# Kernel tuning notes

Measured on AMD Instinct MI355X. Metric: run time of the kernel, lower is better.

The kernel has to match this reference:

```python
import jax, jax.numpy as jnp
import numpy as np

# --- constants from init_kwargs / module defaults ---
H, W, C = 720, 1280, 2
T_EVT, T_PROP = 10, 10
T_TOTAL = T_EVT + T_PROP          # 20 temporal steps (10 event + 10 propagation)
TAU, THR0 = 10.0, 1.0             # LIF time constant, base threshold
ALPHA, TARGET_RATE = 0.1, 0.1     # PENT adaptation
THR_MIN, THR_MAX = 0.1, 10.0
N_EVENTS = 4_000_000


def setup_inputs() -> dict:
    key = jax.random.key(0)
    k1, k2, k3, k4 = jax.random.split(key, 4)
    x = jax.random.randint(k1, (N_EVENTS,), 0, W, dtype=jnp.int32)
    y = jax.random.randint(k2, (N_EVENTS,), 0, H, dtype=jnp.int32)
    p = jax.random.randint(k3, (N_EVENTS,), 0, 2, dtype=jnp.int32)
    t = jax.random.uniform(k4, (N_EVENTS,), dtype=jnp.float32)
    return {"x": x, "y": y, "p": p, "t": t}


def _build_buffer(x, y, p, t):
    # TemporalBuffer.forward: bin events into first T_EVT steps, rest are zeros.
    tmin, tmax = t.min(), t.max()
    denom = jnp.where(tmax > tmin, tmax - tmin, jnp.float32(1.0))
    t_norm = jnp.where(tmax > tmin, (t - tmin) / denom * (T_EVT - 1e-6), 0.0)
    t_idx = jnp.clip(t_norm.astype(jnp.int32), 0, T_EVT - 1)
    xi = jnp.clip(x, 0, W - 1)
    yi = jnp.clip(y, 0, H - 1)
    c_idx = p  # p in {0,1} -> channel index directly (p.min() >= 0 branch)
    buf = jnp.zeros((T_TOTAL, C, H, W), jnp.float32)
    return buf.at[t_idx, c_idx, yi, xi].add(1.0)


def reference(x, y, p, t):
    buffer = _build_buffer(x, y, p, t)  # (T, C, H, W)
    decay = jnp.float32(np.exp(-1.0 / TAU))

    def step(carry, frame):
        mem, thr = carry
        # LIFBuffer: decay + accumulate
        mem = mem * decay + frame
        spk = (mem >= thr).astype(jnp.float32)
        mem = mem - spk * thr  # soft ('subtract') reset
        # AdaptiveThreshold (PENT): homeostatic rate-based adaptation
        rate = spk.mean()
        thr = jnp.clip(thr + ALPHA * (rate - TARGET_RATE), THR_MIN, THR_MAX)
        return (mem, thr), spk

    mem0 = jnp.zeros((C, H, W), jnp.float32)
    (_, _), spikes = jax.lax.scan(step, (mem0, jnp.float32(THR0)), buffer)
    return spikes  # (T, C, H, W) binary spike activity maps
```

## Files before the change

### kernel.cpp

```cpp
#include <hip/hip_runtime.h>
#include <cstddef>

#define HH 720
#define WW 1280
#define FRAME 1843200
#define FRAME4 460800
#define T_EVT 10
#define T_TOTAL 20
#define ARRIVE64 (1ULL << 32)

#define ONBLK 256
#define ONTHR 1024
#define ONWPB 16
#define ONT (ONBLK * ONTHR)

#define SBLK 1024
#define STHR 256
#define SWPB 4
#define PIXB 1800
#define NGROUP4 450
#define HIST_W 9000
#define RBLK 512
#define RTHR 1024
#define OTHR 512
#define NBUCKET 1024
#define BBLK (RBLK / 2)
#define EPT 20
#define MAXM (EPT * RTHR)

#define MAT_OFF   0u
#define CS_OFF    (512u * 1024u * 4u)
#define SB_OFF    (CS_OFF + 4096u)
#define KEY_OFF   (SB_OFF + 8192u)
#define SEG_OFF(n) (KEY_OFF + 4u * (unsigned)(n))
#define WS_NEED(n) ((size_t)SEG_OFF(n) + 2ull * (size_t)(n) + 256ull)

__device__ unsigned g_minkey;
__device__ unsigned g_maxkey;
__device__ unsigned g_part_mn[RBLK];
__device__ unsigned g_part_mx[RBLK];
__device__ unsigned long long g_grp[T_TOTAL][16][16];
__device__ unsigned long long g_top[T_TOTAL][16];
__device__ unsigned g_rel[T_TOTAL][32];
__device__ unsigned long long g_n1[T_TOTAL][64][16];
__device__ unsigned long long g_n2[T_TOTAL][4][16];
__device__ unsigned long long g_n3[T_TOTAL][16];
__device__ unsigned g_relg[T_TOTAL][64][32];

__device__ __forceinline__ unsigned f2key(float f) {
    unsigned b = __float_as_uint(f);
    return b ^ ((unsigned)(((int)b) >> 31) | 0x80000000u);
}
__device__ __forceinline__ float key2f(unsigned k) {
    unsigned b = (k & 0x80000000u) ? (k ^ 0x80000000u) : ~k;
    return __uint_as_float(b);
}

__device__ __forceinline__ int event_bin_t(float tv, float tmin, float tmax) {
#pragma clang fp contract(off)
    float tn;
    if (tmax > tmin) tn = (tv - tmin) / (tmax - tmin) * (float)(10.0 - 1e-6);
    else tn = 0.0f;
    int ti = (int)tn;
    return ti < 0 ? 0 : (ti > T_EVT - 1 ? T_EVT - 1 : ti);
}
__device__ __forceinline__ int event_pixel(int xi, int yi, int ci) {
    xi = xi < 0 ? 0 : (xi > WW - 1 ? WW - 1 : xi);
    yi = yi < 0 ? 0 : (yi > HH - 1 ? HH - 1 : yi);
    return ci * (HH * WW) + yi * WW + xi;
}

__global__ void init_kernel() {
    const int gtid = blockIdx.x * blockDim.x + threadIdx.x;
    const int gs = gridDim.x * blockDim.x;
    if (gtid == 0) { g_minkey = 0xFFFFFFFFu; g_maxkey = 0u; }
    unsigned long long* a = &g_grp[0][0][0];
    for (int i = gtid; i < T_TOTAL * 16 * 16; i += gs) a[i] = 0ull;
    unsigned long long* b = &g_top[0][0];
    for (int i = gtid; i < T_TOTAL * 16; i += gs) b[i] = 0ull;
    unsigned* c = &g_rel[0][0];
    for (int i = gtid; i < T_TOTAL * 32; i += gs) c[i] = 0u;
}

__device__ __forceinline__ void minmax_body(const float* __restrict__ t, int n,
                                            int gtid, int gstride) {
    unsigned mn = 0xFFFFFFFFu, mx = 0u;
    const int n4 = n >> 2;
    const float4* t4 = (const float4*)t;
    for (int i = gtid; i < n4; i += gstride) {
        float4 tv = t4[i];
        unsigned k0 = f2key(tv.x), k1 = f2key(tv.y);
        unsigned k2 = f2key(tv.z), k3 = f2key(tv.w);
        unsigned a = k0 < k1 ? k0 : k1, b = k2 < k3 ? k2 : k3;
        unsigned c = a < b ? a : b;
        mn = mn < c ? mn : c;
        a = k0 > k1 ? k0 : k1; b = k2 > k3 ? k2 : k3;
        c = a > b ? a : b;
        mx = mx > c ? mx : c;
    }
    for (int i = (n4 << 2) + gtid; i < n; i += gstride) {
        unsigned k = f2key(t[i]);
        mn = mn < k ? mn : k;
        mx = mx > k ? mx : k;
    }
    for (int off = 32; off > 0; off >>= 1) {
        unsigned omn = (unsigned)__shfl_down((int)mn, off, 64);
        unsigned omx = (unsigned)__shfl_down((int)mx, off, 64);
        mn = mn < omn ? mn : omn;
        mx = mx > omx ? mx : omx;
    }
    __shared__ unsigned smn[16], smx[16];
    int lane = threadIdx.x & 63, wv = threadIdx.x >> 6;
    if (lane == 0) { smn[wv] = mn; smx[wv] = mx; }
    __syncthreads();
    if (threadIdx.x == 0) {
        int nw = blockDim.x >> 6;
        for (int i = 1; i < nw; ++i) {
            mn = mn < smn[i] ? mn : smn[i];
            mx = mx > smx[i] ? mx : smx[i];
        }
        atomicMin(&g_minkey, mn);
        atomicMax(&g_maxkey, mx);
    }
}

__global__ void minmax_zero_kernel(const float* __restrict__ t, int n,
                                   uint4* __restrict__ hist16v) {
    const int gtid = blockIdx.x * blockDim.x + threadIdx.x;
    const int gstride = gridDim.x * blockDim.x;
    const uint4 z = make_uint4(0u, 0u, 0u, 0u);
    const int nz = T_EVT * FRAME / 8;
    for (int i = gtid; i < nz; i += gstride) hist16v[i] = z;
    minmax_body(t, n, gtid, gstride);
}

__global__ __launch_bounds__(RTHR) void passA_kernel(
        const int* __restrict__ x, const int* __restrict__ y,
        const int* __restrict__ p, const float* __restrict__ t,
        unsigned* __restrict__ mat, unsigned* __restrict__ keys, int n) {
    __shared__ unsigned cnt[NBUCKET];
    const int gtid = blockIdx.x * blockDim.x + threadIdx.x;
    const int gs = gridDim.x * blockDim.x;
    {
        unsigned long long* z1 = &g_n1[0][0][0];
        for (int i = gtid; i < T_TOTAL * 64 * 16; i += gs) z1[i] = 0ull;
        unsigned long long* z2 = &g_n2[0][0][0];
        for (int i = gtid; i < T_TOTAL * 4 * 16; i += gs) z2[i] = 0ull;
        unsigned long long* z3 = &g_n3[0][0];
        for (int i = gtid; i < T_TOTAL * 16; i += gs) z3[i] = 0ull;
        unsigned* z4 = &g_relg[0][0][0];
        for (int i = gtid; i < T_TOTAL * 64 * 32; i += gs) z4[i] = 0u;
    }
    for (int i = threadIdx.x; i < NBUCKET; i += blockDim.x) cnt[i] = 0u;
    __syncthreads();
    const int chunk = (n + RBLK - 1) / RBLK;
    const int s0 = blockIdx.x * chunk;
    const int s1 = min(n, s0 + chunk);
    unsigned mn = 0xFFFFFFFFu, mx = 0u;
    for (int i = s0 + threadIdx.x; i < s1; i += blockDim.x) {
        int pix = event_pixel(x[i], y[i], p[i]);
        keys[i] = (unsigned)pix;
        atomicAdd(&cnt[pix / PIXB], 1u);
        unsigned k = f2key(t[i]);
        mn = mn < k ? mn : k;
        mx = mx > k ? mx : k;
    }
    for (int off = 32; off > 0; off >>= 1) {
        unsigned omn = (unsigned)__shfl_down((int)mn, off, 64);
        unsigned omx = (unsigned)__shfl_down((int)mx, off, 64);
        mn = mn < omn ? mn : omn;
        mx = mx > omx ? mx : omx;
    }
    __shared__ unsigned smn[RTHR / 64], smx[RTHR / 64];
    const int lane = threadIdx.x & 63, wv = threadIdx.x >> 6;
    if (lane == 0) { smn[wv] = mn; smx[wv] = mx; }
    __syncthreads();
    if (threadIdx.x == 0) {
#pragma unroll
        for (int i = 1; i < RTHR / 64; ++i) {
            mn = mn < smn[i] ? mn : smn[i];
            mx = mx > smx[i] ? mx : smx[i];
        }
        g_part_mn[blockIdx.x] = mn;
        g_part_mx[blockIdx.x] = mx;
    }
    for (int i = threadIdx.x; i < NBUCKET; i += blockDim.x)
        mat[blockIdx.x * NBUCKET + i] = cnt[i];
}

__global__ __launch_bounds__(OTHR) void offsets_col_kernel(
        unsigned* __restrict__ mat, unsigned* __restrict__ colsum) {
    const int j = blockIdx.x;
    const int r = threadIdx.x;
    const int lane = r & 63, wv = r >> 6;
    unsigned v = mat[r * NBUCKET + j];
    unsigned incl = v;
    for (int off = 1; off < 64; off <<= 1) {
        unsigned o = (unsigned)__shfl_up((int)incl, off, 64);
        if (lane >= off) incl += o;
    }
    __shared__ unsigned wtot[OTHR / 64];
    if (lane == 63) wtot[wv] = incl;
    __syncthreads();
    if (r == 0) {
        unsigned run = 0;
#pragma unroll
        for (int k = 0; k < OTHR / 64; ++k) { unsigned tmp = wtot[k]; wtot[k] = run; run += tmp; }
    }
    __syncthreads();
    unsigned ex = incl - v + wtot[wv];
    mat[r * NBUCKET + j] = ex;
    if (r == OTHR - 1) colsum[j] = ex + v;

    if (j == 0) {
        unsigned mn = g_part_mn[r], mx = g_part_mx[r];
        for (int off = 32; off > 0; off >>= 1) {
            unsigned omn = (unsigned)__shfl_down((int)mn, off, 64);
            unsigned omx = (unsigned)__shfl_down((int)mx, off, 64);
            mn = mn < omn ? mn : omn;
            mx = mx > omx ? mx : omx;
        }
        __shared__ unsigned smn2[OTHR / 64], smx2[OTHR / 64];
        if (lane == 0) { smn2[wv] = mn; smx2[wv] = mx; }
        __syncthreads();
        if (r == 0) {
#pragma unroll
            for (int k = 1; k < OTHR / 64; ++k) {
                mn = mn < smn2[k] ? mn : smn2[k];
                mx = mx > smx2[k] ? mx : smx2[k];
            }
            g_minkey = mn;
            g_maxkey = mx;
        }
    }
}

__global__ __launch_bounds__(RTHR) void passB_kernel(
        const unsigned* __restrict__ keys, const float* __restrict__ t,
        const unsigned* __restrict__ mat, const unsigned* __restrict__ colsum,
        unsigned* __restrict__ seg_base_out,
        unsigned short* __restrict__ seg, int n) {
    __shared__ unsigned base[NBUCKET];
    __shared__ unsigned lrun[NBUCKET];
    __shared__ unsigned wt2[RTHR / 64];
    __shared__ unsigned short sorted[MAXM];
    __shared__ unsigned short sbkt[MAXM];
    const int j = threadIdx.x;
    const int lane = j & 63, wv = j >> 6;
    {
        unsigned v = colsum[j];
        unsigned incl = v;
        for (int off = 1; off < 64; off <<= 1) {
            unsigned o = (unsigned)__shfl_up((int)incl, off, 64);
            if (lane >= off) incl += o;
        }
        if (lane == 63) wt2[wv] = incl;
        __syncthreads();
        if (j == 0) {
            unsigned run = 0;
#pragma unroll
            for (int k = 0; k < RTHR / 64; ++k) { unsigned tmp = wt2[k]; wt2[k] = run; run += tmp; }
        }
        __syncthreads();
        unsigned ex = incl - v + wt2[wv];
        base[j] = mat[(2 * blockIdx.x) * NBUCKET + j] + ex;
        lrun[j] = 0u;
        if (blockIdx.x == 0) {
            seg_base_out[j] = ex;
            if (j == NBUCKET - 1) seg_base_out[NBUCKET] = ex + v;
        }
    }
    __syncthreads();
    const float tmin = key2f(g_minkey);
    const float tmax = key2f(g_maxkey);
    const int cA = (n + RBLK - 1) / RBLK;
    const int s0 = blockIdx.x * 2 * cA;
    const int s1 = min(n, s0 + 2 * cA);
    const int m = s1 - s0;

    unsigned rec[EPT];
#pragma unroll
    for (int k = 0; k < EPT; ++k) {
        rec[k] = 0xFFFFFFFFu;
        int i = s0 + k * RTHR + j;
        if (i < s1) {
            int pix = (int)keys[i];
            int ti = event_bin_t(t[i], tmin, tmax);
            int bkt = pix / PIXB;
            int lb = ti * PIXB + (pix - bkt * PIXB);
            rec[k] = ((unsigned)bkt << 16) | (unsigned)lb;
            atomicAdd(&lrun[bkt], 1u);
        }
    }
    __syncthreads();
    {
        unsigned v = lrun[j];
        unsigned incl = v;
        for (int off = 1; off < 64; off <<= 1) {
            unsigned o = (unsigned)__shfl_up((int)incl, off, 64);
            if (lane >= off) incl += o;
        }
        if (lane == 63) wt2[wv] = incl;
        __syncthreads();
        if (j == 0) {
            unsigned run = 0;
#pragma unroll
            for (int k = 0; k < RTHR / 64; ++k) { unsigned tmp = wt2[k]; wt2[k] = run; run += tmp; }
        }
        __syncthreads();
        unsigned ex = incl - v + wt2[wv];
        base[j] -= ex;
        lrun[j] = ex;
    }
    __syncthreads();
#pragma unroll
    for (int k = 0; k < EPT; ++k) {
        unsigned r0 = rec[k];
        if (r0 != 0xFFFFFFFFu) {
            unsigned bkt = r0 >> 16;
            unsigned r = atomicAdd(&lrun[bkt], 1u);
            sorted[r] = (unsigned short)(r0 & 0xFFFFu);
            sbkt[r] = (unsigned short)bkt;
        }
    }
    __syncthreads();
    for (int i = j; i < m; i += RTHR) {
        unsigned bk = sbkt[i];
        seg[base[bk] + (unsigned)i] = sorted[i];
    }
}

__global__ __launch_bounds__(STHR, 4) void scan_new(float* __restrict__ out,
                                                    const unsigned short* __restrict__ seg,
                                                    const unsigned* __restrict__ seg_base) {
#pragma clang fp contract(off)
    const float decay = (float)0.9048374180359595;
    const int tid = threadIdx.x;
    const int lane = tid & 63;
    const int b = blockIdx.x;
    const int pix0 = b * PIXB;

    __shared__ alignas(16) unsigned lds_hist[HIST_W];
    __shared__ unsigned lds_arr[T_TOTAL];
    __shared__ unsigned lds_tot[T_TOTAL];

    for (int i = tid; i < HIST_W; i += STHR) lds_hist[i] = 0u;
    if (tid < T_TOTAL) { lds_arr[tid] = 0u; lds_tot[tid] = 0u; }
    __syncthreads();

    {
        const int e0 = (int)seg_base[b];
        const int e1 = (int)seg_base[b + 1];
        for (int i = e0 + tid; i < e1; i += STHR) {
            unsigned lb = seg[i];
            atomicAdd(&lds_hist[lb >> 1], 1u << ((lb & 1u) << 4));
        }
    }
    __syncthreads();

    const bool has1 = tid < (NGROUP4 - STHR);
    float4 mem0 = make_float4(0.f, 0.f, 0.f, 0.f);
    float4 mem1 = make_float4(0.f, 0.f, 0.f, 0.f);
    float thr = 1.0f;

    float4 f0, f1;
    {
        uint2 w01 = *(const uint2*)&lds_hist[tid << 1];
        f0 = make_float4((float)(w01.x & 0xFFFFu), (float)(w01.x >> 16),
                         (float)(w01.y & 0xFFFFu), (float)(w01.y >> 16));
        if (has1) {
            uint2 v = *(const uint2*)&lds_hist[(tid + STHR) << 1];
            f1 = make_float4((float)(v.x & 0xFFFFu), (float)(v.x >> 16),
                             (float)(v.y & 0xFFFFu), (float)(v.y >> 16));
        } else f1 = make_float4(0.f, 0.f, 0.f, 0.f);
    }

    for (int s = 0;; ++s) {
        float* ob = out + (size_t)s * FRAME + pix0;
        int cnt = 0;

        {
            float4 m, spk;
            m.x = mem0.x + f0.x;
            m.y = mem0.y + f0.y;
            m.z = mem0.z + f0.z;
            m.w = mem0.w + f0.w;
            spk.x = (m.x >= thr) ? 1.0f : 0.0f;
            spk.y = (m.y >= thr) ? 1.0f : 0.0f;
            spk.z = (m.z >= thr) ? 1.0f : 0.0f;
            spk.w = (m.w >= thr) ? 1.0f : 0.0f;
            ((float4*)ob)[tid] = spk;
            mem0.x = m.x - spk.x * thr;
            mem0.y = m.y - spk.y * thr;
            mem0.z = m.z - spk.z * thr;
            mem0.w = m.w - spk.w * thr;
            cnt += (int)spk.x + (int)spk.y + (int)spk.z + (int)spk.w;
        }
        if (has1) {
            int g = tid + STHR;
            float4 m, spk;
            m.x = mem1.x + f1.x;
            m.y = mem1.y + f1.y;
            m.z = mem1.z + f1.z;
            m.w = mem1.w + f1.w;
            spk.x = (m.x >= thr) ? 1.0f : 0.0f;
            spk.y = (m.y >= thr) ? 1.0f : 0.0f;
            spk.z = (m.z >= thr) ? 1.0f : 0.0f;
            spk.w = (m.w >= thr) ? 1.0f : 0.0f;
            ((float4*)ob)[g] = spk;
            mem1.x = m.x - spk.x * thr;
            mem1.y = m.y - spk.y * thr;
            mem1.z = m.z - spk.z * thr;
            mem1.w = m.w - spk.w * thr;
            cnt += (int)spk.x + (int)spk.y + (int)spk.z + (int)spk.w;
        }

        if (s == T_TOTAL - 1) break;

        for (int off = 32; off > 0; off >>= 1) cnt += __shfl_down(cnt, off, 64);

        bool last = false;
        const int g1 = b >> 4;
        if (lane == 0) {
            unsigned old = __hip_atomic_fetch_add(&lds_arr[s],
                               (unsigned)cnt + (1u << 16),
                               __ATOMIC_RELAXED, __HIP_MEMORY_SCOPE_WORKGROUP);
            if ((old >> 16) == SWPB - 1) {
                last = true;
                unsigned bc = (old + (unsigned)cnt) & 0xFFFFu;
                unsigned long long a1 = __hip_atomic_fetch_add(
                    &g_n1[s][g1][0], (unsigned long long)bc + ARRIVE64,
                    __ATOMIC_RELAXED, __HIP_MEMORY_SCOPE_AGENT);
                if ((unsigned)(a1 >> 32) == 15u) {
                    unsigned c1 = (unsigned)a1 + bc;
                    const int g2 = g1 >> 4;
                    unsigned long long a2 = __hip_atomic_fetch_add(
                        &g_n2[s][g2][0], (unsigned long long)c1 + ARRIVE64,
                        __ATOMIC_RELAXED, __HIP_MEMORY_SCOPE_AGENT);
                    if ((unsigned)(a2 >> 32) == 15u) {
                        unsigned c2 = (unsigned)a2 + c1;
                        unsigned long long a3 = __hip_atomic_fetch_add(
                            &g_n3[s][0], (unsigned long long)c2 + ARRIVE64,
                            __ATOMIC_RELAXED, __HIP_MEMORY_SCOPE_AGENT);
                        if ((unsigned)(a3 >> 32) == 3u) {
                            unsigned tot = (unsigned)a3 + c2;
                            for (int g = 0; g < 64; ++g)
                                __hip_atomic_store(&g_relg[s][g][0], tot + 1u,
                                    __ATOMIC_RELAXED, __HIP_MEMORY_SCOPE_AGENT);
                        }
                    }
                }
            }
        }

        {
            const int sn = s + 1;
            if (sn < T_EVT) {
                uint2 w01 = *(const uint2*)&lds_hist[sn * 900 + (tid << 1)];
                f0 = make_float4((float)(w01.x & 0xFFFFu), (float)(w01.x >> 16),
                                 (float)(w01.y & 0xFFFFu), (float)(w01.y >> 16));
                if (has1) {
                    uint2 v = *(const uint2*)&lds_hist[sn * 900 + ((tid + STHR) << 1)];
                    f1 = make_float4((float)(v.x & 0xFFFFu), (float)(v.x >> 16),
                                     (float)(v.y & 0xFFFFu), (float)(v.y >> 16));
                }
            } else {
                f0 = make_float4(0.f, 0.f, 0.f, 0.f);
                f1 = make_float4(0.f, 0.f, 0.f, 0.f);
            }
            mem0.x = mem0.x * decay; mem0.y = mem0.y * decay;
            mem0.z = mem0.z * decay; mem0.w = mem0.w * decay;
            mem1.x = mem1.x * decay; mem1.y = mem1.y * decay;
            mem1.z = mem1.z * decay; mem1.w = mem1.w * decay;
        }
        __builtin_amdgcn_sched_barrier(0);

        unsigned total = 0u;
        if (lane == 0) {
            unsigned f;
            if (last) {
                do {
                    __builtin_amdgcn_s_sleep(1);
                    f = __hip_atomic_load(&g_relg[s][g1][0], __ATOMIC_RELAXED,
                                          __HIP_MEMORY_SCOPE_AGENT);
                } while (f == 0u);
                total = f - 1u;
                __hip_atomic_store(&lds_tot[s], f,
                                   __ATOMIC_RELAXED, __HIP_MEMORY_SCOPE_WORKGROUP);
            } else {
                unsigned f2;
                do {
                    __builtin_amdgcn_s_sleep(1);
                    f2 = __hip_atomic_load(&lds_tot[s], __ATOMIC_RELAXED,
                                           __HIP_MEMORY_SCOPE_WORKGROUP);
                } while (f2 == 0u);
                total = f2 - 1u;
            }
        }
        total = (unsigned)__shfl((int)total, 0, 64);
        float rate = (float)total / 1843200.0f;
        thr = thr + 0.1f * (rate - 0.1f);
        thr = fminf(fmaxf(thr, 0.1f), 10.0f);
    }
}

__global__ void scatter_kernel(const int* __restrict__ x, const int* __restrict__ y,
                               const int* __restrict__ p, const float* __restrict__ t,
                               unsigned* __restrict__ hist32, int n) {
    int i = blockIdx.x * blockDim.x + threadIdx.x;
    if (i >= n) return;
    float tmin = key2f(g_minkey);
    float tmax = key2f(g_maxkey);
    int ti = event_bin_t(t[i], tmin, tmax);
    int pix = event_pixel(x[i], y[i], p[i]);
    size_t bidx = (size_t)ti * FRAME + pix;
    atomicAdd(hist32 + (bidx >> 1), 1u << ((bidx & 1) << 4));
}

__global__ __launch_bounds__(ONTHR) void scan_old(float* __restrict__ out) {
#pragma clang fp contract(off)
    const float decay = (float)0.9048374180359595;
    const int gtid = blockIdx.x * ONTHR + threadIdx.x;
    const int lane = threadIdx.x & 63;
    const uint2 uz2 = make_uint2(0u, 0u);
    float4 mem0 = make_float4(0.f, 0.f, 0.f, 0.f);
    float4 mem1 = make_float4(0.f, 0.f, 0.f, 0.f);
    const bool has1 = (gtid + ONT) < FRAME4;
    float thr = 1.0f;
    const uint2* hist2 = (const uint2*)(out + (size_t)T_EVT * FRAME);
    __shared__ unsigned lds_arr[T_TOTAL];
    __shared__ unsigned lds_tot[T_TOTAL];
    if (threadIdx.x < T_TOTAL) { lds_arr[threadIdx.x] = 0u; lds_tot[threadIdx.x] = 0u; }
    __syncthreads();
    uint2 u0 = hist2[gtid];
    uint2 u1 = has1 ? hist2[gtid + ONT] : uz2;
    for (int s = 0; s < T_TOTAL; ++s) {
        float4* o4 = (float4*)(out + (size_t)s * FRAME);
        int cnt = 0;
        {
            float4 m, spk;
            m.x = mem0.x * decay; m.x = m.x + (float)(u0.x & 0xFFFFu);
            m.y = mem0.y * decay; m.y = m.y + (float)(u0.x >> 16);
            m.z = mem0.z * decay; m.z = m.z + (float)(u0.y & 0xFFFFu);
            m.w = mem0.w * decay; m.w = m.w + (float)(u0.y >> 16);
            spk.x = (m.x >= thr) ? 1.0f : 0.0f;
            spk.y = (m.y >= thr) ? 1.0f : 0.0f;
            spk.z = (m.z >= thr) ? 1.0f : 0.0f;
            spk.w = (m.w >= thr) ? 1.0f : 0.0f;
            o4[gtid] = spk;
            mem0.x = m.x - spk.x * thr; mem0.y = m.y - spk.y * thr;
            mem0.z = m.z - spk.z * thr; mem0.w = m.w - spk.w * thr;
            cnt += (int)spk.x + (int)spk.y + (int)spk.z + (int)spk.w;
        }
        if (has1) {
            float4 m, spk;
            m.x = mem1.x * decay; m.x = m.x + (float)(u1.x & 0xFFFFu);
            m.y = mem1.y * decay; m.y = m.y + (float)(u1.x >> 16);
            m.z = mem1.z * decay; m.z = m.z + (float)(u1.y & 0xFFFFu);
            m.w = mem1.w * decay; m.w = m.w + (float)(u1.y >> 16);
            spk.x = (m.x >= thr) ? 1.0f : 0.0f;
            spk.y = (m.y >= thr) ? 1.0f : 0.0f;
            spk.z = (m.z >= thr) ? 1.0f : 0.0f;
            spk.w = (m.w >= thr) ? 1.0f : 0.0f;
            o4[gtid + ONT] = spk;
            mem1.x = m.x - spk.x * thr; mem1.y = m.y - spk.y * thr;
            mem1.z = m.z - spk.z * thr; mem1.w = m.w - spk.w * thr;
            cnt += (int)spk.x + (int)spk.y + (int)spk.z + (int)spk.w;
        }
        if (s + 1 < T_EVT) {
            const uint2* hn = hist2 + (size_t)(s + 1) * FRAME4;
            u0 = hn[gtid];
            u1 = has1 ? hn[gtid + ONT] : uz2;
        } else { u0 = uz2; u1 = uz2; }
        if (s == T_TOTAL - 1) break;
        for (int off = 32; off > 0; off >>= 1) cnt += __shfl_down(cnt, off, 64);
        unsigned total = 0u;
        if (lane == 0) {
            unsigned old = __hip_atomic_fetch_add(&lds_arr[s],
                               (unsigned)cnt + (1u << 16),
                               __ATOMIC_RELAXED, __HIP_MEMORY_SCOPE_WORKGROUP);
            if ((old >> 16) == ONWPB - 1) {
                unsigned bc = (old + (unsigned)cnt) & 0xFFFFu;
                const int gid = blockIdx.x >> 4;
                unsigned long long gold = __hip_atomic_fetch_add(
                    &g_grp[s][gid][0], (unsigned long long)bc + ARRIVE64,
                    __ATOMIC_RELAXED, __HIP_MEMORY_SCOPE_AGENT);
                if ((unsigned)(gold >> 32) == 15u) {
                    unsigned gc = (unsigned)gold + bc;
                    unsigned long long told = __hip_atomic_fetch_add(
                        &g_top[s][0], (unsigned long long)gc + ARRIVE64,
                        __ATOMIC_RELAXED, __HIP_MEMORY_SCOPE_AGENT);
                    if ((unsigned)(told >> 32) == 15u) {
                        unsigned tot = (unsigned)told + gc;
                        __hip_atomic_store(&g_rel[s][0], tot + 1u,
                                           __ATOMIC_RELAXED, __HIP_MEMORY_SCOPE_AGENT);
                    }
                }
                unsigned f;
                do {
                    __builtin_amdgcn_s_sleep(1);
                    f = __hip_atomic_load(&g_rel[s][0], __ATOMIC_RELAXED,
                                          __HIP_MEMORY_SCOPE_AGENT);
                } while (f == 0u);
                total = f - 1u;
                __hip_atomic_store(&lds_tot[s], f,
                                   __ATOMIC_RELAXED, __HIP_MEMORY_SCOPE_WORKGROUP);
            } else {
                unsigned f;
                do {
                    __builtin_amdgcn_s_sleep(1);
                    f = __hip_atomic_load(&lds_tot[s], __ATOMIC_RELAXED,
                                          __HIP_MEMORY_SCOPE_WORKGROUP);
                } while (f == 0u);
                total = f - 1u;
            }
        }
        total = (unsigned)__shfl((int)total, 0, 64);
        float rate = (float)total / 1843200.0f;
        thr = thr + 0.1f * (rate - 0.1f);
        thr = fminf(fmaxf(thr, 0.1f), 10.0f);
    }
}

extern "C" void kernel_launch(void* const* d_in, const int* in_sizes, int n_in,
                              void* d_out, int out_size, void* d_ws, size_t ws_size,
                              hipStream_t stream) {
    const int*   x = (const int*)d_in[0];
    const int*   y = (const int*)d_in[1];
    const int*   p = (const int*)d_in[2];
    const float* t = (const float*)d_in[3];
    float* out = (float*)d_out;
    const int n = in_sizes[0];

    const int cA = (n + RBLK - 1) / RBLK;
    if (d_ws != nullptr && ws_size >= WS_NEED(n) && 2 * cA <= MAXM) {
        unsigned* mat = (unsigned*)((char*)d_ws + MAT_OFF);
        unsigned* colsum = (unsigned*)((char*)d_ws + CS_OFF);
        unsigned* seg_base = (unsigned*)((char*)d_ws + SB_OFF);
        unsigned* keys = (unsigned*)((char*)d_ws + KEY_OFF);
        unsigned short* seg = (unsigned short*)((char*)d_ws + SEG_OFF(n));

        passA_kernel<<<RBLK, RTHR, 0, stream>>>(x, y, p, t, mat, keys, n);
        offsets_col_kernel<<<NBUCKET, OTHR, 0, stream>>>(mat, colsum);
        passB_kernel<<<BBLK, RTHR, 0, stream>>>(keys, t, mat, colsum, seg_base, seg, n);

        dim3 g(SBLK), b(STHR);
        void* args[] = { (void*)&out, (void*)&seg, (void*)&seg_base };
        hipLaunchCooperativeKernel((void*)scan_new, g, b, args, 0, stream);
    } else {
        init_kernel<<<64, 256, 0, stream>>>();
        unsigned* hist32 = (unsigned*)(out + (size_t)T_EVT * FRAME);
        minmax_zero_kernel<<<1024, 256, 0, stream>>>(t, n, (uint4*)hist32);
        scatter_kernel<<<(n + 255) / 256, 256, 0, stream>>>(x, y, p, t, hist32, n);
        dim3 g(ONBLK), b(ONTHR);
        void* args[] = { (void*)&out };
        hipLaunchCooperativeKernel((void*)scan_old, g, b, args, 0, stream);
    }
}
```

Measured before the change: 321.7 us.

## Match passB blocks to passA chunks and rewrite offsets scan as coalesced row-group scan

```diff
diff --git a/kernel.cpp b/kernel.cpp
--- a/kernel.cpp
+++ b/kernel.cpp
@@ -22,11 +22,12 @@
 #define HIST_W 9000
 #define RBLK 512
 #define RTHR 1024
-#define OTHR 512
 #define NBUCKET 1024
-#define BBLK (RBLK / 2)
-#define EPT 20
+#define EPT 8
 #define MAXM (EPT * RTHR)
+#define OBLK 16
+#define OROWG 16
+#define OROWS 32
 
 #define MAT_OFF   0u
 #define CS_OFF    (512u * 1024u * 4u)
@@ -188,44 +189,53 @@
         mat[blockIdx.x * NBUCKET + i] = cnt[i];
 }
 
-__global__ __launch_bounds__(OTHR) void offsets_col_kernel(
+__global__ __launch_bounds__(1024) void offsets_kernel(
         unsigned* __restrict__ mat, unsigned* __restrict__ colsum) {
-    const int j = blockIdx.x;
-    const int r = threadIdx.x;
-    const int lane = r & 63, wv = r >> 6;
-    unsigned v = mat[r * NBUCKET + j];
-    unsigned incl = v;
-    for (int off = 1; off < 64; off <<= 1) {
-        unsigned o = (unsigned)__shfl_up((int)incl, off, 64);
-        if (lane >= off) incl += o;
-    }
-    __shared__ unsigned wtot[OTHR / 64];
-    if (lane == 63) wtot[wv] = incl;
-    __syncthreads();
-    if (r == 0) {
-        unsigned run = 0;
+    const int t = threadIdx.x;
+    const int c = t & 63;
+    const int rg = t >> 6;
+    const int j = blockIdx.x * 64 + c;
+    __shared__ unsigned part[OROWG][64];
+    unsigned sum = 0u;
+    for (int k = 0; k < OROWS; ++k)
+        sum += mat[(rg * OROWS + k) * NBUCKET + j];
+    part[rg][c] = sum;
+    __syncthreads();
+    if (rg == 0) {
+        unsigned run = 0u;
 #pragma unroll
-        for (int k = 0; k < OTHR / 64; ++k) { unsigned tmp = wtot[k]; wtot[k] = run; run += tmp; }
-    }
-    __syncthreads();
-    unsigned ex = incl - v + wtot[wv];
-    mat[r * NBUCKET + j] = ex;
-    if (r == OTHR - 1) colsum[j] = ex + v;
-
-    if (j == 0) {
-        unsigned mn = g_part_mn[r], mx = g_part_mx[r];
+        for (int g = 0; g < OROWG; ++g) {
+            unsigned v = part[g][c];
+            part[g][c] = run;
+            run += v;
+        }
+        colsum[j] = run;
+    }
+    __syncthreads();
+    unsigned running = part[rg][c];
+    for (int k = 0; k < OROWS; ++k) {
+        const int idx = (rg * OROWS + k) * NBUCKET + j;
+        unsigned v = mat[idx];
+        mat[idx] = running;
+        running += v;
+    }
+
+    if (blockIdx.x == 0) {
+        const int lane = t & 63, wv = t >> 6;
+        unsigned mn = 0xFFFFFFFFu, mx = 0u;
+        if (t < RBLK) { mn = g_part_mn[t]; mx = g_part_mx[t]; }
         for (int off = 32; off > 0; off >>= 1) {
             unsigned omn = (unsigned)__shfl_down((int)mn, off, 64);
             unsigned omx = (unsigned)__shfl_down((int)mx, off, 64);
             mn = mn < omn ? mn : omn;
             mx = mx > omx ? mx : omx;
         }
-        __shared__ unsigned smn2[OTHR / 64], smx2[OTHR / 64];
+        __shared__ unsigned smn2[16], smx2[16];
         if (lane == 0) { smn2[wv] = mn; smx2[wv] = mx; }
         __syncthreads();
-        if (r == 0) {
+        if (t == 0) {
 #pragma unroll
-            for (int k = 1; k < OTHR / 64; ++k) {
+            for (int k = 1; k < 16; ++k) {
                 mn = mn < smn2[k] ? mn : smn2[k];
                 mx = mx > smx2[k] ? mx : smx2[k];
             }
@@ -263,7 +273,7 @@
         }
         __syncthreads();
         unsigned ex = incl - v + wt2[wv];
-        base[j] = mat[(2 * blockIdx.x) * NBUCKET + j] + ex;
+        base[j] = mat[blockIdx.x * NBUCKET + j] + ex;
         lrun[j] = 0u;
         if (blockIdx.x == 0) {
             seg_base_out[j] = ex;
@@ -273,9 +283,9 @@
     __syncthreads();
     const float tmin = key2f(g_minkey);
     const float tmax = key2f(g_maxkey);
-    const int cA = (n + RBLK - 1) / RBLK;
-    const int s0 = blockIdx.x * 2 * cA;
-    const int s1 = min(n, s0 + 2 * cA);
+    const int chunk = (n + RBLK - 1) / RBLK;
+    const int s0 = blockIdx.x * chunk;
+    const int s1 = min(n, s0 + chunk);
     const int m = s1 - s0;
 
     unsigned rec[EPT];
@@ -632,8 +642,8 @@
     float* out = (float*)d_out;
     const int n = in_sizes[0];
 
-    const int cA = (n + RBLK - 1) / RBLK;
-    if (d_ws != nullptr && ws_size >= WS_NEED(n) && 2 * cA <= MAXM) {
+    const int chunk = (n + RBLK - 1) / RBLK;
+    if (d_ws != nullptr && ws_size >= WS_NEED(n) && chunk <= MAXM) {
         unsigned* mat = (unsigned*)((char*)d_ws + MAT_OFF);
         unsigned* colsum = (unsigned*)((char*)d_ws + CS_OFF);
         unsigned* seg_base = (unsigned*)((char*)d_ws + SB_OFF);
@@ -641,8 +651,8 @@
         unsigned short* seg = (unsigned short*)((char*)d_ws + SEG_OFF(n));
 
         passA_kernel<<<RBLK, RTHR, 0, stream>>>(x, y, p, t, mat, keys, n);
-        offsets_col_kernel<<<NBUCKET, OTHR, 0, stream>>>(mat, colsum);
-        passB_kernel<<<BBLK, RTHR, 0, stream>>>(keys, t, mat, colsum, seg_base, seg, n);
+        offsets_kernel<<<OBLK, 1024, 0, stream>>>(mat, colsum);
+        passB_kernel<<<RBLK, RTHR, 0, stream>>>(keys, t, mat, colsum, seg_base, seg, n);
 
         dim3 g(SBLK), b(STHR);
         void* args[] = { (void*)&out, (void*)&seg, (void*)&seg_base };
```

New measurement: 309.2 us. 1.04x faster.
